# Optimization experiments

Hardware: AMD Instinct MI355X
Metric: run time of the kernel (lower is better)

## Reference

```python
import jax, jax.numpy as jnp
import numpy as np

B, T, C = 2, 2048, 1024
N_HEAD = 16
HEAD_DIM = C // N_HEAD
N_WORLDS = 4


def setup_inputs() -> dict:
    key = jax.random.key(0)
    kx, kq, kk, kv, kp, ka = jax.random.split(key, 6)
    scale = 0.02
    x = jax.random.normal(kx, (B, T, C), dtype=jnp.float32)
    Wq = jax.random.normal(kq, (C, C), dtype=jnp.float32) * scale
    Wk = jax.random.normal(kk, (C, C), dtype=jnp.float32) * scale
    Wv = jax.random.normal(kv, (C, C), dtype=jnp.float32) * scale
    Wproj = jax.random.normal(kp, (C, C), dtype=jnp.float32) * scale
    acc = jax.random.randint(ka, (N_WORLDS, N_WORLDS), 0, 2, dtype=jnp.int32)
    # ensure every world accesses itself so no softmax row is fully masked
    acc = acc.at[jnp.arange(N_WORLDS), jnp.arange(N_WORLDS)].set(1)
    return {"x": x, "Wq": Wq, "Wk": Wk, "Wv": Wv, "Wproj": Wproj,
            "accessibility": acc}


def reference(x, Wq, Wk, Wv, Wproj, accessibility):
    Bd, Td, Cd = x.shape
    # torch Linear: y = x @ W.T  -> project then split heads
    q = (x @ Wq.T).reshape(Bd, Td, N_HEAD, HEAD_DIM).transpose(0, 2, 1, 3)
    k = (x @ Wk.T).reshape(Bd, Td, N_HEAD, HEAD_DIM).transpose(0, 2, 1, 3)
    v = (x @ Wv.T).reshape(Bd, Td, N_HEAD, HEAD_DIM).transpose(0, 2, 1, 3)

    scores = jnp.einsum('bhqd,bhkd->bhqk', q, k) / jnp.sqrt(
        jnp.asarray(HEAD_DIM, dtype=x.dtype))

    # Kripke modal mask: token t lives in world t % n_worlds (necessity: \u25a1)
    world = jnp.arange(Td) % accessibility.shape[0]
    modal_mask = accessibility[world][:, world]          # (T, T) 0/1
    scores = jnp.where(modal_mask[None, None] == 0, -jnp.inf, scores)

    attn = jax.nn.softmax(scores, axis=-1)
    out = jnp.einsum('bhqk,bhkd->bhqd', attn, v)
    out = out.transpose(0, 2, 1, 3).reshape(Bd, Td, Cd)
    return out @ Wproj.T
```

## Files before the change

### kernel.cpp

```cpp
#include <hip/hip_runtime.h>
#include <hip/hip_bf16.h>
#include <stdint.h>


typedef __attribute__((ext_vector_type(8))) __bf16   bf16x8;
typedef __attribute__((ext_vector_type(4))) float    f32x4;
typedef __attribute__((ext_vector_type(8))) ushort   ushort8;

__device__ __forceinline__ ushort f2bf(float x) {
    uint32_t u = __float_as_uint(x);
    return (ushort)((u + 0x7fffu + ((u >> 16) & 1u)) >> 16);
}
__device__ __forceinline__ float sentinel(float v, float s) {
    return (fabsf(v) < 1e30f) ? v : s;
}
__device__ __forceinline__ f32x4 mfma16(bf16x8 a, bf16x8 b, f32x4 c) {
    return __builtin_amdgcn_mfma_f32_16x16x32_bf16(a, b, c, 0, 0, 0);
}
__device__ __forceinline__ ushort2 pk2(float a, float b) {
    __hip_bfloat162 h = __float22bfloat162_rn(make_float2(a, b));
    union { __hip_bfloat162 h; ushort2 u; } c; c.h = h; return c.u;
}
__device__ __forceinline__ ushort4 cvt4(float4 v) {
    ushort2 lo = pk2(v.x, v.y), hi = pk2(v.z, v.w);
    ushort4 r; r.x = lo.x; r.y = lo.y; r.z = hi.x; r.w = hi.y; return r;
}
__device__ __forceinline__ ushort4 cvt4s(float4 v, float s) {
    ushort2 lo = pk2(v.x * s, v.y * s), hi = pk2(v.z * s, v.w * s);
    ushort4 r; r.x = lo.x; r.y = lo.y; r.z = hi.x; r.w = hi.y; return r;
}
__device__ __forceinline__ float fexp2(float x) {
#if __has_builtin(__builtin_amdgcn_exp2f)
    return __builtin_amdgcn_exp2f(x);
#else
    return exp2f(x);
#endif
}
__device__ __forceinline__ void gld16(const ushort* g, ushort* l) {
    auto* g1 = reinterpret_cast<const __attribute__((address_space(1))) uint32_t*>(
        reinterpret_cast<uintptr_t>(g));
    auto* l3 = reinterpret_cast<__attribute__((address_space(3))) uint32_t*>(
        reinterpret_cast<uintptr_t>(l));
    __builtin_amdgcn_global_load_lds(g1, l3, 16, 0, 0);
}

__device__ __forceinline__ int swz(int row, int ch) {
    return row * 64 + ((ch ^ (row & 7)) * 8);
}

__device__ __forceinline__ int wperm(int ts) {
    return ((ts & 3) << 9) | (ts >> 2);
}

__device__ __forceinline__ int vshuf(int r) {
    return ((r & 31) << 2) | (r >> 5);
}
__device__ __forceinline__ int vshufX(int r) {
    return ((r & 63) << 2) | (r >> 6);
}

#define QSCALE 0.1803368801111244f

__global__ __launch_bounds__(256) void cvt_prepass(
        const float* __restrict__ x,  const float* __restrict__ Wq,
        const float* __restrict__ Wk, const float* __restrict__ Wv,
        const float* __restrict__ Wp,
        ushort* __restrict__ xb,  ushort* __restrict__ wqb,
        ushort* __restrict__ wkb, ushort* __restrict__ wvb,
        ushort* __restrict__ wpb)
{
    int gid = blockIdx.x;
    const float* src; ushort* dst; float sc = 1.0f; int boff;
    if (gid < 4096)      { src = x;  dst = xb;  boff = gid; }
    else if (gid < 5120) { src = Wq; dst = wqb; boff = gid - 4096; sc = QSCALE; }
    else if (gid < 6144) { src = Wk; dst = wkb; boff = gid - 5120; }
    else if (gid < 7168) { src = Wv; dst = wvb; boff = gid - 6144; }
    else                 { src = Wp; dst = wpb; boff = gid - 7168; }
    size_t idx = (size_t)boff * 1024 + threadIdx.x * 4;
    float4 v = *(const float4*)&src[idx];
    *(ushort4*)&dst[idx] = cvt4s(v, sc);
}

__global__ __launch_bounds__(512, 2) void gemm_qkv_b(
        const ushort* __restrict__ xb,
        const ushort* __restrict__ wqb, const ushort* __restrict__ wkb,
        const ushort* __restrict__ wvb,
        ushort* __restrict__ Cq, ushort* __restrict__ Ck,
        ushort* __restrict__ Cv)
{
    __shared__ ushort As[2][256 * 32];
    __shared__ ushort Bs[2][256 * 32];

    const int tid  = threadIdx.x;
    const int lane = tid & 63;
    const int wave = tid >> 6;
    const int quad = lane >> 4;
    const int l15  = lane & 15;
    const int wm2  = wave >> 2;
    const int wn4  = wave & 3;

    const int bid = blockIdx.x;
    const bool isV = bid >= 128;
    int tokb, chO;
    const ushort* __restrict__ Aw;
    ushort* __restrict__ C;
    if (!isV) {
        const int blkM = bid & 7;
        const int blkN = bid >> 3;
        tokb = blkN * 256;
        const int chb2 = blkM * 256;
        chO  = chb2 & 1023;
        Aw = (blkM < 4) ? (wqb + (size_t)chb2 * 1024)
                        : (wkb + (size_t)(chb2 - 1024) * 1024);
        C  = (blkM < 4) ? Cq : Ck;
    } else {
        const int v = bid - 128;
        tokb = (v & 15) * 256;
        chO  = (v >> 4) * 256;
        Aw = wvb + (size_t)chO * 1024;
        C  = Cv;
    }

    auto stage = [&](int kt, int buf) {
        const int kcol = kt * 32;
        #pragma unroll
        for (int j = 0; j < 2; ++j) {
            int ci = j * 512 + tid;
            int r  = ci >> 2;
            int qc = (((ci & 3) ^ (r & 3) ^ ((r >> 2) & 3))) * 8;
            const ushort* asrc = isV ? &xb[(size_t)(tokb + vshufX(r)) * 1024]
                                     : &Aw[(size_t)r * 1024];
            const ushort* bsrc = isV ? &Aw[(size_t)r * 1024]
                                     : &xb[(size_t)(tokb + r) * 1024];
            gld16(&asrc[kcol + qc], &As[buf][ci * 8]);
            gld16(&bsrc[kcol + qc], &Bs[buf][ci * 8]);
        }
    };

    f32x4 acc[8][4] = {};

    stage(0, 0);
    for (int t = 0; t < 32; ++t) {
        const int cur = t & 1;
        __syncthreads();
        if (t < 31) stage(t + 1, cur ^ 1);

        bf16x8 af[8], bf[4];
        #pragma unroll
        for (int i = 0; i < 8; ++i) {
            int row = wm2 * 128 + i * 16 + l15;
            int pos = quad ^ (row & 3) ^ ((row >> 2) & 3);
            af[i] = *(const bf16x8*)&As[cur][row * 32 + pos * 8];
        }
        #pragma unroll
        for (int tt = 0; tt < 4; ++tt) {
            int row = wn4 * 64 + tt * 16 + l15;
            int pos = quad ^ (row & 3) ^ ((row >> 2) & 3);
            bf[tt] = *(const bf16x8*)&Bs[cur][row * 32 + pos * 8];
        }
        #pragma unroll
        for (int i = 0; i < 8; ++i)
            #pragma unroll
            for (int tt = 0; tt < 4; ++tt)
                acc[i][tt] = mfma16(af[i], bf[tt], acc[i][tt]);
    }

    if (!isV) {
        #pragma unroll
        for (int i = 0; i < 8; ++i) {
            int ch = chO + wm2 * 128 + i * 16 + quad * 4;
            int hh = ch >> 6, d0 = ch & 63;
            #pragma unroll
            for (int tt = 0; tt < 4; ++tt) {
                int n = tokb + wn4 * 64 + tt * 16 + l15;
                int b = n >> 11, ts = n & 2047;
                ushort4 hv;
                hv.x = f2bf(sentinel(acc[i][tt][0], 1e8f));
                hv.y = f2bf(sentinel(acc[i][tt][1], 1e8f));
                hv.z = f2bf(sentinel(acc[i][tt][2], 1e8f));
                hv.w = f2bf(sentinel(acc[i][tt][3], 1e8f));
                *(ushort4*)&C[((size_t)((b << 4) | hh) * 2048 + wperm(ts)) * 64 + d0] = hv;
            }
        }
    } else {
        const int b = tokb >> 11;
        #pragma unroll
        for (int i = 0; i < 8; ++i) {
            int mi0 = wm2 * 128 + i * 16 + quad * 4;
            int colbase = ((mi0 >> 6) << 9) + ((tokb & 2047) >> 2) + (mi0 & 63);
            #pragma unroll
            for (int tt = 0; tt < 4; ++tt) {
                int n = chO + wn4 * 64 + tt * 16 + l15;
                int hh = n >> 6, d = n & 63;
                ushort4 hv;
                hv.x = f2bf(sentinel(acc[i][tt][0], 1e8f));
                hv.y = f2bf(sentinel(acc[i][tt][1], 1e8f));
                hv.z = f2bf(sentinel(acc[i][tt][2], 1e8f));
                hv.w = f2bf(sentinel(acc[i][tt][3], 1e8f));
                *(ushort4*)&C[((size_t)((b << 4) | hh) * 64 + d) * 2048 + colbase] = hv;
            }
        }
    }
}

__global__ __launch_bounds__(256) void gemm_proj_b(
        const ushort* __restrict__ O, const ushort* __restrict__ wpb,
        float* __restrict__ out)
{
    __shared__ ushort As[128 * 64];
    __shared__ ushort Bs[64 * 64];

    const int lin  = blockIdx.x + 16 * blockIdx.y;
    const int xcd  = lin & 7;
    const int slot = lin >> 3;
    const int bx   = (xcd & 1) * 8 + (slot % 8);
    const int by   = (xcd >> 1) * 8 + (slot / 8);

    const int tid  = threadIdx.x;
    const int lane = tid & 63;
    const int wave = tid >> 6;
    const int quad = lane >> 4;
    const int l15  = lane & 15;
    const int bm = by * 128, bn = bx * 64;
    const int wm = (wave & 1) * 64,  wn = (wave >> 1) * 32;

    f32x4 acc[4][2] = {};

    for (int k0 = 0; k0 < 1024; k0 += 64) {
        __syncthreads();
        int h = k0 >> 6;
        #pragma unroll
        for (int j = 0; j < 4; ++j) {
            int cb = j * 256 + wave * 64;
            int ci = cb + lane;
            int r  = ci >> 3;
            int qc = (ci & 7) ^ (r & 7);
            int m = bm + r;
            int b = m >> 11, ts = m & 2047;
            gld16(&O[((((size_t)(b * 16 + h)) * 2048 + wperm(ts)) << 6) + qc * 8],
                  &As[cb * 8]);
        }
        #pragma unroll
        for (int j = 0; j < 2; ++j) {
            int cb = j * 256 + wave * 64;
            int ci = cb + lane;
            int r  = ci >> 3;
            int qc = (ci & 7) ^ (r & 7);
            gld16(&wpb[(size_t)(bn + r) * 1024 + k0 + qc * 8], &Bs[cb * 8]);
        }
        __syncthreads();

        bf16x8 af[2][4], bfr[2][2];
        #pragma unroll
        for (int f = 0; f < 2; ++f) {
            int ch = f * 4 + quad;
            #pragma unroll
            for (int i = 0; i < 4; ++i)
                af[f][i] = *(const bf16x8*)&As[swz(wm + i * 16 + l15, ch)];
            #pragma unroll
            for (int t = 0; t < 2; ++t)
                bfr[f][t] = *(const bf16x8*)&Bs[swz(wn + t * 16 + l15, ch)];
        }
        #pragma unroll
        for (int f = 0; f < 2; ++f)
            #pragma unroll
            for (int i = 0; i < 4; ++i)
                #pragma unroll
                for (int t = 0; t < 2; ++t)
                    acc[i][t] = mfma16(af[f][i], bfr[f][t], acc[i][t]);
    }

    #pragma unroll
    for (int i = 0; i < 4; ++i)
        #pragma unroll
        for (int t = 0; t < 2; ++t)
            #pragma unroll
            for (int r = 0; r < 4; ++r) {
                int m = bm + wm + i * 16 + quad * 4 + r;
                int n = bn + wn + t * 16 + l15;
                out[(size_t)m * 1024 + n] = sentinel(acc[i][t][r], 100.0f);
            }
}

__global__ __launch_bounds__(256) void attn_kernel(
        ushort* __restrict__ Q, const ushort* __restrict__ Kk,
        const ushort* __restrict__ Vt_g, const int* __restrict__ accm)
{
    __shared__ ushort Ks[2][64 * 64];
    __shared__ ushort Vt[2][64 * 64];
    __shared__ ushort Ps[4][32 * 64];

    const int tid  = threadIdx.x;
    const int lane = tid & 63;
    const int wave = tid >> 6;
    const int quad = lane >> 4;
    const int l15  = lane & 15;
    const int bh = blockIdx.x, qt = blockIdx.y;

    ushort*       Qg = Q    + ((size_t)bh * 2048 + qt * 128) * 64;
    const ushort* Kg = Kk   + (size_t)bh * 2048 * 64;
    const ushort* Vg = Vt_g + (size_t)bh * 64 * 2048;

    const int qworld = qt >> 2;
    int gpack = 0, ng = 0;
    #pragma unroll
    for (int w = 0; w < 4; ++w)
        if (accm[qworld * 4 + w] != 0) { gpack |= w << (ng * 8); ++ng; }
    const int nkt = ng * 8;
    auto ktof = [&](int i) {
        return ((((gpack >> ((i >> 3) << 3)) & 3) << 3) | (i & 7));
    };

    bf16x8 aq[2][2];
    #pragma unroll
    for (int i = 0; i < 2; ++i)
        #pragma unroll
        for (int f = 0; f < 2; ++f)
            aq[i][f] = *(const bf16x8*)
                &Qg[(wave * 32 + i * 16 + l15) * 64 + f * 32 + quad * 8];

    bf16x8 aones;
    #pragma unroll
    for (int j = 0; j < 8; ++j) aones[j] = (__bf16)1.0f;

    f32x4 oacc[4][2] = {};
    f32x4 lacc[2] = {};

    auto stage = [&](int kt, int buf) {
        #pragma unroll
        for (int j = 0; j < 2; ++j) {
            int cb = j * 256 + wave * 64;
            int ci = cb + lane;
            int r  = ci >> 3;
            int qc = (ci & 7) ^ (r & 7);
            gld16(&Kg[((size_t)kt * 64 + r) * 64 + qc * 8], &Ks[buf][cb * 8]);
            gld16(&Vg[(size_t)r * 2048 + kt * 64 + qc * 8], &Vt[buf][cb * 8]);
        }
    };

    stage(ktof(0), 0);
    for (int it = 0; it < nkt; ++it) {
        const int cur = it & 1;
        __syncthreads();
        if (it < nkt - 1) stage(ktof(it + 1), cur ^ 1);

        f32x4 st[4][2] = {};
        #pragma unroll
        for (int f = 0; f < 2; ++f) {
            int ch = f * 4 + quad;
            #pragma unroll
            for (int k4 = 0; k4 < 4; ++k4) {
                bf16x8 ak = *(const bf16x8*)&Ks[cur][swz(k4 * 16 + l15, ch)];
                #pragma unroll
                for (int i = 0; i < 2; ++i)
                    st[k4][i] = mfma16(ak, aq[i][f], st[k4][i]);
            }
        }

        #pragma unroll
        for (int i = 0; i < 2; ++i) {
            int prow = i * 16 + l15;
            #pragma unroll
            for (int k4 = 0; k4 < 4; ++k4) {
                float p0 = fexp2(st[k4][i][0]);
                float p1 = fexp2(st[k4][i][1]);
                float p2 = fexp2(st[k4][i][2]);
                float p3 = fexp2(st[k4][i][3]);
                ushort2 lo = pk2(p0, p1), hi = pk2(p2, p3);
                ushort4 pv4; pv4.x = lo.x; pv4.y = lo.y;
                pv4.z = hi.x; pv4.w = hi.y;
                int pc8 = (k4 * 2 + (quad >> 1)) ^ (l15 & 7);
                *(ushort4*)&Ps[wave][prow * 64 + pc8 * 8 + (quad & 1) * 4] = pv4;
            }
        }

        bf16x8 bp[2][2];
        #pragma unroll
        for (int i = 0; i < 2; ++i)
            #pragma unroll
            for (int f = 0; f < 2; ++f)
                bp[i][f] = *(const bf16x8*)&Ps[wave][swz(i * 16 + l15, f * 4 + quad)];
        #pragma unroll
        for (int f = 0; f < 2; ++f) {
            int ch = f * 4 + quad;
            #pragma unroll
            for (int i = 0; i < 2; ++i)
                lacc[i] = mfma16(aones, bp[i][f], lacc[i]);
            #pragma unroll
            for (int dt = 0; dt < 4; ++dt) {
                bf16x8 av = *(const bf16x8*)&Vt[cur][swz(dt * 16 + l15, ch)];
                #pragma unroll
                for (int i = 0; i < 2; ++i)
                    oacc[dt][i] = mfma16(av, bp[i][f], oacc[dt][i]);
            }
        }
    }

    #pragma unroll
    for (int i = 0; i < 2; ++i) {
        const float inv = 1.0f / lacc[i][0];
        #pragma unroll
        for (int dt = 0; dt < 4; ++dt) {
            ushort4 o4;
            o4.x = f2bf(sentinel(oacc[dt][i][0] * inv, 1e4f));
            o4.y = f2bf(sentinel(oacc[dt][i][1] * inv, 1e4f));
            o4.z = f2bf(sentinel(oacc[dt][i][2] * inv, 1e4f));
            o4.w = f2bf(sentinel(oacc[dt][i][3] * inv, 1e4f));
            *(ushort4*)&Qg[(wave * 32 + i * 16 + l15) * 64 + dt * 16 + quad * 4] = o4;
        }
    }
}

__global__ __launch_bounds__(256) void gemm_qkv_f32(
        const float* __restrict__ A,
        const float* __restrict__ Wq, const float* __restrict__ Wk,
        const float* __restrict__ Wv,
        ushort* __restrict__ Cq, ushort* __restrict__ Ck,
        ushort* __restrict__ Cv)
{
    __shared__ __align__(16) ushort As[128 * 72];
    __shared__ __align__(16) ushort Bs[128 * 72];

    const int sel = blockIdx.x >> 3;
    const float* __restrict__ Bw = sel == 0 ? Wq : (sel == 1 ? Wk : Wv);
    ushort* __restrict__ C       = sel == 0 ? Cq : (sel == 1 ? Ck : Cv);
    const float scale = sel == 0 ? QSCALE : 1.0f;

    const int tid  = threadIdx.x;
    const int lane = tid & 63;
    const int wave = tid >> 6;
    const int quad = lane >> 4;
    const int l15  = lane & 15;
    const int bm = blockIdx.y * 128;
    const int bn = (blockIdx.x & 7) * 128;
    const int wm = (wave & 1) * 64, wn = (wave >> 1) * 64;

    f32x4 acc[4][4] = {};

    for (int k0 = 0; k0 < 1024; k0 += 64) {
        __syncthreads();
        #pragma unroll
        for (int i = 0; i < 8; ++i) {
            int c = tid + 256 * i;
            int row = c >> 4, col = (c & 15) * 4;
            int rg = (sel == 2) ? vshuf(row) : row;
            float4 a4 = *(const float4*)&A[(size_t)(bm + rg) * 1024 + k0 + col];
            *(ushort4*)&As[row * 72 + col] = cvt4(a4);
            float4 b4 = *(const float4*)&Bw[(size_t)(bn + row) * 1024 + k0 + col];
            *(ushort4*)&Bs[row * 72 + col] = cvt4s(b4, scale);
        }
        __syncthreads();

        bf16x8 af[2][4], bfr[2][4];
        #pragma unroll
        for (int f = 0; f < 2; ++f)
            #pragma unroll
            for (int i = 0; i < 4; ++i) {
                af[f][i]  = *(const bf16x8*)&As[(wm + i * 16 + l15) * 72 + f * 32 + quad * 8];
                bfr[f][i] = *(const bf16x8*)&Bs[(wn + i * 16 + l15) * 72 + f * 32 + quad * 8];
            }
        #pragma unroll
        for (int f = 0; f < 2; ++f)
            #pragma unroll
            for (int i = 0; i < 4; ++i)
                #pragma unroll
                for (int t = 0; t < 4; ++t)
                    acc[i][t] = mfma16(af[f][i], bfr[f][t], acc[i][t]);
    }

    if (sel < 2) {
        #pragma unroll
        for (int i = 0; i < 4; ++i)
            #pragma unroll
            for (int t = 0; t < 4; ++t)
                #pragma unroll
                for (int r = 0; r < 4; ++r) {
                    int m = bm + wm + i * 16 + quad * 4 + r;
                    int n = bn + wn + t * 16 + l15;
                    int b = m >> 11, ts = m & 2047, hh = n >> 6, d = n & 63;
                    C[((size_t)((b << 4) | hh) * 2048 + wperm(ts)) * 64 + d] =
                        f2bf(sentinel(acc[i][t][r], 1e8f));
                }
    } else {
        const int b = bm >> 11;
        #pragma unroll
        for (int i = 0; i < 4; ++i) {
            int mi0 = wm + i * 16 + quad * 4;
            int colbase = ((mi0 >> 5) << 9) + ((bm & 2047) >> 2) + (mi0 & 31);
            #pragma unroll
            for (int t = 0; t < 4; ++t) {
                int n = bn + wn + t * 16 + l15;
                int hh = n >> 6, d = n & 63;
                ushort4 hv;
                hv.x = f2bf(sentinel(acc[i][t][0], 1e8f));
                hv.y = f2bf(sentinel(acc[i][t][1], 1e8f));
                hv.z = f2bf(sentinel(acc[i][t][2], 1e8f));
                hv.w = f2bf(sentinel(acc[i][t][3], 1e8f));
                *(ushort4*)&C[((size_t)((b << 4) | hh) * 64 + d) * 2048 + colbase] = hv;
            }
        }
    }
}

__global__ __launch_bounds__(256) void gemm_proj_f32(
        const ushort* __restrict__ A, const float* __restrict__ Bw,
        float* __restrict__ C)
{
    __shared__ __align__(16) ushort As[128 * 72];
    __shared__ __align__(16) ushort Bs[64 * 72];

    const int tid  = threadIdx.x;
    const int lane = tid & 63;
    const int wave = tid >> 6;
    const int quad = lane >> 4;
    const int l15  = lane & 15;
    const int bm = blockIdx.y * 128, bn = blockIdx.x * 64;
    const int wm = (wave & 1) * 64,  wn = (wave >> 1) * 32;

    f32x4 acc[4][2] = {};

    for (int k0 = 0; k0 < 1024; k0 += 64) {
        __syncthreads();
        #pragma unroll
        for (int i = 0; i < 4; ++i) {
            int c = tid + 256 * i;
            int row = c >> 3, col = (c & 7) * 8;
            int m = bm + row;
            int b = m >> 11, ts = m & 2047, h = k0 >> 6;
            size_t aoff = ((((size_t)(b * 16 + h)) * 2048 + wperm(ts)) << 6) + col;
            *(ushort8*)&As[row * 72 + col] = *(const ushort8*)&A[aoff];
        }
        #pragma unroll
        for (int i = 0; i < 4; ++i) {
            int c = tid + 256 * i;
            int row = c >> 4, col = (c & 15) * 4;
            float4 b4 = *(const float4*)&Bw[(size_t)(bn + row) * 1024 + k0 + col];
            *(ushort4*)&Bs[row * 72 + col] = cvt4(b4);
        }
        __syncthreads();

        bf16x8 af[2][4], bfr[2][2];
        #pragma unroll
        for (int f = 0; f < 2; ++f) {
            #pragma unroll
            for (int i = 0; i < 4; ++i)
                af[f][i] = *(const bf16x8*)&As[(wm + i * 16 + l15) * 72 + f * 32 + quad * 8];
            #pragma unroll
            for (int t = 0; t < 2; ++t)
                bfr[f][t] = *(const bf16x8*)&Bs[(wn + t * 16 + l15) * 72 + f * 32 + quad * 8];
        }
        #pragma unroll
        for (int f = 0; f < 2; ++f)
            #pragma unroll
            for (int i = 0; i < 4; ++i)
                #pragma unroll
                for (int t = 0; t < 2; ++t)
                    acc[i][t] = mfma16(af[f][i], bfr[f][t], acc[i][t]);
    }

    #pragma unroll
    for (int i = 0; i < 4; ++i)
        #pragma unroll
        for (int t = 0; t < 2; ++t)
            #pragma unroll
            for (int r = 0; r < 4; ++r) {
                int m = bm + wm + i * 16 + quad * 4 + r;
                int n = bn + wn + t * 16 + l15;
                C[(size_t)m * 1024 + n] = sentinel(acc[i][t][r], 100.0f);
            }
}

__global__ void diag_kernel(float* out, int n, float val) {
    int i = blockIdx.x * blockDim.x + threadIdx.x;
    if (i < n) out[i] = (i == 0) ? val : 0.f;
}

extern "C" void kernel_launch(void* const* d_in, const int* in_sizes, int n_in,
                              void* d_out, int out_size, void* d_ws, size_t ws_size,
                              hipStream_t stream) {
    const float* x  = (const float*)d_in[0];
    const float* Wq = (const float*)d_in[1];
    const float* Wk = (const float*)d_in[2];
    const float* Wv = (const float*)d_in[3];
    const float* Wp = (const float*)d_in[4];
    const int* accm = (const int*)d_in[5];
    float* out = (float*)d_out;

    const size_t SZ = (size_t)4 * 1024 * 1024;
    const size_t WSZ = (size_t)1024 * 1024;

    if (ws_size < 3 * SZ * sizeof(ushort)) {
        diag_kernel<<<(out_size + 255) / 256, 256, 0, stream>>>(
            out, out_size, (float)ws_size);
        return;
    }

    ushort* k_ws = (ushort*)d_ws;
    ushort* v_ws = k_ws + SZ;
    ushort* q_ws = v_ws + SZ;
    dim3 blk(256);

    const size_t need_fast = (4 * SZ + 4 * WSZ) * sizeof(ushort);
    if (ws_size >= need_fast) {
        ushort* xb  = q_ws + SZ;
        ushort* wqb = xb + SZ;
        ushort* wkb = wqb + WSZ;
        ushort* wvb = wkb + WSZ;
        ushort* wpb = wvb + WSZ;
        cvt_prepass<<<8192, blk, 0, stream>>>(x, Wq, Wk, Wv, Wp,
                                              xb, wqb, wkb, wvb, wpb);
        gemm_qkv_b<<<dim3(192), dim3(512), 0, stream>>>(xb, wqb, wkb, wvb,
                                                        q_ws, k_ws, v_ws);
        attn_kernel<<<dim3(32, 16), blk, 0, stream>>>(q_ws, k_ws, v_ws, accm);
        gemm_proj_b<<<dim3(16, 32), blk, 0, stream>>>(q_ws, wpb, out);
    } else {
        gemm_qkv_f32<<<dim3(24, 32), blk, 0, stream>>>(x, Wq, Wk, Wv,
                                                       q_ws, k_ws, v_ws);
        attn_kernel<<<dim3(32, 16), blk, 0, stream>>>(q_ws, k_ws, v_ws, accm);
        gemm_proj_f32<<<dim3(16, 32), blk, 0, stream>>>(q_ws, Wp, out);
    }
}
```

Measured before the change: 163.6 us.

## Triple-buffer QKV GEMM with 64-wide K tiles and swap proj GEMM operands

The QKV GEMM now uses 256x128 output tiles with 64-wide K steps and a three-stage LDS ring, using explicit vmcnt waits, raw barriers and setprio instead of a double-buffered __syncthreads loop. The grid doubles to 384 blocks to improve CU occupancy, at the cost of more LDS per block (about 144KB) and more redundant operand loads. The projection GEMM swaps the A/B roles so each lane writes contiguous float4 chunks of the output instead of scalar stores. The LDS footprint may limit the launch bound of two blocks per CU.

```diff
diff --git a/kernel.cpp b/kernel.cpp
--- a/kernel.cpp
+++ b/kernel.cpp
@@ -88,8 +88,8 @@
         ushort* __restrict__ Cq, ushort* __restrict__ Ck,
         ushort* __restrict__ Cv)
 {
-    __shared__ ushort As[2][256 * 32];
-    __shared__ ushort Bs[2][256 * 32];
+    __shared__ ushort As[3][256 * 64];
+    __shared__ ushort Bs[3][128 * 64];
 
     const int tid  = threadIdx.x;
     const int lane = tid & 63;
@@ -100,69 +100,91 @@
     const int wn4  = wave & 3;
 
     const int bid = blockIdx.x;
-    const bool isV = bid >= 128;
+    const bool isV = bid >= 256;
     int tokb, chO;
-    const ushort* __restrict__ Aw;
+    const ushort* __restrict__ Asrc;
+    const ushort* __restrict__ Bsrc;
     ushort* __restrict__ C;
     if (!isV) {
         const int blkM = bid & 7;
         const int blkN = bid >> 3;
-        tokb = blkN * 256;
+        tokb = blkN * 128;
         const int chb2 = blkM * 256;
         chO  = chb2 & 1023;
-        Aw = (blkM < 4) ? (wqb + (size_t)chb2 * 1024)
-                        : (wkb + (size_t)(chb2 - 1024) * 1024);
-        C  = (blkM < 4) ? Cq : Ck;
+        Asrc = (blkM < 4) ? (wqb + (size_t)chb2 * 1024)
+                          : (wkb + (size_t)(chb2 - 1024) * 1024);
+        Bsrc = xb;
+        C    = (blkM < 4) ? Cq : Ck;
     } else {
-        const int v = bid - 128;
-        tokb = (v & 15) * 256;
-        chO  = (v >> 4) * 256;
-        Aw = wvb + (size_t)chO * 1024;
-        C  = Cv;
+        const int v = bid - 256;
+        const int blkVn = v & 7;
+        tokb = (v >> 3) * 256;
+        chO  = blkVn * 128;
+        Asrc = xb;
+        Bsrc = wvb + (size_t)chO * 1024;
+        C    = Cv;
     }
 
     auto stage = [&](int kt, int buf) {
-        const int kcol = kt * 32;
+        const int kcol = kt * 64;
+        #pragma unroll
+        for (int j = 0; j < 4; ++j) {
+            int ci = j * 512 + tid;
+            int r  = ci >> 3;
+            int qc = ((ci & 7) ^ (r & 7)) * 8;
+            int rg = isV ? (tokb + vshufX(r)) : r;
+            const ushort* src = isV ? &Asrc[(size_t)rg * 1024]
+                                    : &Asrc[(size_t)r * 1024];
+            gld16(&src[kcol + qc], &As[buf][ci * 8]);
+        }
         #pragma unroll
         for (int j = 0; j < 2; ++j) {
             int ci = j * 512 + tid;
-            int r  = ci >> 2;
-            int qc = (((ci & 3) ^ (r & 3) ^ ((r >> 2) & 3))) * 8;
-            const ushort* asrc = isV ? &xb[(size_t)(tokb + vshufX(r)) * 1024]
-                                     : &Aw[(size_t)r * 1024];
-            const ushort* bsrc = isV ? &Aw[(size_t)r * 1024]
-                                     : &xb[(size_t)(tokb + r) * 1024];
-            gld16(&asrc[kcol + qc], &As[buf][ci * 8]);
-            gld16(&bsrc[kcol + qc], &Bs[buf][ci * 8]);
+            int r  = ci >> 3;
+            int qc = ((ci & 7) ^ (r & 7)) * 8;
+            const ushort* src = isV ? &Bsrc[(size_t)r * 1024]
+                                    : &Bsrc[(size_t)(tokb + r) * 1024];
+            gld16(&src[kcol + qc], &Bs[buf][ci * 8]);
         }
     };
 
-    f32x4 acc[8][4] = {};
+    f32x4 acc[8][2] = {};
 
     stage(0, 0);
-    for (int t = 0; t < 32; ++t) {
-        const int cur = t & 1;
-        __syncthreads();
-        if (t < 31) stage(t + 1, cur ^ 1);
-
-        bf16x8 af[8], bf[4];
-        #pragma unroll
-        for (int i = 0; i < 8; ++i) {
-            int row = wm2 * 128 + i * 16 + l15;
-            int pos = quad ^ (row & 3) ^ ((row >> 2) & 3);
-            af[i] = *(const bf16x8*)&As[cur][row * 32 + pos * 8];
-        }
-        #pragma unroll
-        for (int tt = 0; tt < 4; ++tt) {
-            int row = wn4 * 64 + tt * 16 + l15;
-            int pos = quad ^ (row & 3) ^ ((row >> 2) & 3);
-            bf[tt] = *(const bf16x8*)&Bs[cur][row * 32 + pos * 8];
-        }
-        #pragma unroll
-        for (int i = 0; i < 8; ++i)
-            #pragma unroll
-            for (int tt = 0; tt < 4; ++tt)
-                acc[i][tt] = mfma16(af[i], bf[tt], acc[i][tt]);
+    stage(1, 1);
+    asm volatile("s_waitcnt vmcnt(6)" ::: "memory");
+    __builtin_amdgcn_s_barrier();
+    __builtin_amdgcn_sched_barrier(0);
+
+    for (int t = 0; t < 16; ++t) {
+        const int cur = t % 3;
+        if (t + 2 < 16) stage(t + 2, (t + 2) % 3);
+
+        __builtin_amdgcn_s_setprio(1);
+        #pragma unroll
+        for (int f = 0; f < 2; ++f) {
+            int ch = f * 4 + quad;
+            bf16x8 af[8], bfv[2];
+            #pragma unroll
+            for (int i = 0; i < 8; ++i)
+                af[i] = *(const bf16x8*)&As[cur][swz(wm2 * 128 + i * 16 + l15, ch)];
+            #pragma unroll
+            for (int tt = 0; tt < 2; ++tt)
+                bfv[tt] = *(const bf16x8*)&Bs[cur][swz(wn4 * 32 + tt * 16 + l15, ch)];
+            #pragma unroll
+            for (int i = 0; i < 8; ++i)
+                #pragma unroll
+                for (int tt = 0; tt < 2; ++tt)
+                    acc[i][tt] = mfma16(af[i], bfv[tt], acc[i][tt]);
+        }
+        __builtin_amdgcn_s_setprio(0);
+
+        if (t < 15) {
+            if (t < 14) asm volatile("s_waitcnt vmcnt(6)" ::: "memory");
+            else        asm volatile("s_waitcnt vmcnt(0)" ::: "memory");
+            __builtin_amdgcn_s_barrier();
+            __builtin_amdgcn_sched_barrier(0);
+        }
     }
 
     if (!isV) {
@@ -171,8 +193,8 @@
             int ch = chO + wm2 * 128 + i * 16 + quad * 4;
             int hh = ch >> 6, d0 = ch & 63;
             #pragma unroll
-            for (int tt = 0; tt < 4; ++tt) {
-                int n = tokb + wn4 * 64 + tt * 16 + l15;
+            for (int tt = 0; tt < 2; ++tt) {
+                int n = tokb + wn4 * 32 + tt * 16 + l15;
                 int b = n >> 11, ts = n & 2047;
                 ushort4 hv;
                 hv.x = f2bf(sentinel(acc[i][tt][0], 1e8f));
@@ -189,8 +211,8 @@
             int mi0 = wm2 * 128 + i * 16 + quad * 4;
             int colbase = ((mi0 >> 6) << 9) + ((tokb & 2047) >> 2) + (mi0 & 63);
             #pragma unroll
-            for (int tt = 0; tt < 4; ++tt) {
-                int n = chO + wn4 * 64 + tt * 16 + l15;
+            for (int tt = 0; tt < 2; ++tt) {
+                int n = chO + wn4 * 32 + tt * 16 + l15;
                 int hh = n >> 6, d = n & 63;
                 ushort4 hv;
                 hv.x = f2bf(sentinel(acc[i][tt][0], 1e8f));
@@ -207,8 +229,8 @@
         const ushort* __restrict__ O, const ushort* __restrict__ wpb,
         float* __restrict__ out)
 {
-    __shared__ ushort As[128 * 64];
-    __shared__ ushort Bs[64 * 64];
+    __shared__ ushort As[64 * 64];
+    __shared__ ushort Bs[128 * 64];
 
     const int lin  = blockIdx.x + 16 * blockIdx.y;
     const int xcd  = lin & 7;
@@ -221,65 +243,69 @@
     const int wave = tid >> 6;
     const int quad = lane >> 4;
     const int l15  = lane & 15;
-    const int bm = by * 128, bn = bx * 64;
-    const int wm = (wave & 1) * 64,  wn = (wave >> 1) * 32;
-
-    f32x4 acc[4][2] = {};
+    const int chb = bx * 64, tokb = by * 128;
+    const int wm = (wave & 1) * 32,  wn = (wave >> 1) * 64;
+
+    f32x4 acc[2][4] = {};
 
     for (int k0 = 0; k0 < 1024; k0 += 64) {
         __syncthreads();
         int h = k0 >> 6;
+        #pragma unroll
+        for (int j = 0; j < 2; ++j) {
+            int cb = j * 256 + wave * 64;
+            int ci = cb + lane;
+            int r  = ci >> 3;
+            int qc = (ci & 7) ^ (r & 7);
+            gld16(&wpb[(size_t)(chb + r) * 1024 + k0 + qc * 8], &As[cb * 8]);
+        }
         #pragma unroll
         for (int j = 0; j < 4; ++j) {
             int cb = j * 256 + wave * 64;
             int ci = cb + lane;
             int r  = ci >> 3;
             int qc = (ci & 7) ^ (r & 7);
-            int m = bm + r;
+            int m = tokb + r;
             int b = m >> 11, ts = m & 2047;
             gld16(&O[((((size_t)(b * 16 + h)) * 2048 + wperm(ts)) << 6) + qc * 8],
-                  &As[cb * 8]);
-        }
-        #pragma unroll
-        for (int j = 0; j < 2; ++j) {
-            int cb = j * 256 + wave * 64;
-            int ci = cb + lane;
-            int r  = ci >> 3;
-            int qc = (ci & 7) ^ (r & 7);
-            gld16(&wpb[(size_t)(bn + r) * 1024 + k0 + qc * 8], &Bs[cb * 8]);
+                  &Bs[cb * 8]);
         }
         __syncthreads();
 
-        bf16x8 af[2][4], bfr[2][2];
+        bf16x8 af[2][2], bfr[2][4];
         #pragma unroll
         for (int f = 0; f < 2; ++f) {
             int ch = f * 4 + quad;
             #pragma unroll
-            for (int i = 0; i < 4; ++i)
+            for (int i = 0; i < 2; ++i)
                 af[f][i] = *(const bf16x8*)&As[swz(wm + i * 16 + l15, ch)];
             #pragma unroll
-            for (int t = 0; t < 2; ++t)
+            for (int t = 0; t < 4; ++t)
                 bfr[f][t] = *(const bf16x8*)&Bs[swz(wn + t * 16 + l15, ch)];
         }
         #pragma unroll
         for (int f = 0; f < 2; ++f)
             #pragma unroll
-            for (int i = 0; i < 4; ++i)
+            for (int i = 0; i < 2; ++i)
                 #pragma unroll
-                for (int t = 0; t < 2; ++t)
+                for (int t = 0; t < 4; ++t)
                     acc[i][t] = mfma16(af[f][i], bfr[f][t], acc[i][t]);
     }
 
     #pragma unroll
-    for (int i = 0; i < 4; ++i)
-        #pragma unroll
-        for (int t = 0; t < 2; ++t)
-            #pragma unroll
-            for (int r = 0; r < 4; ++r) {
-                int m = bm + wm + i * 16 + quad * 4 + r;
-                int n = bn + wn + t * 16 + l15;
-                out[(size_t)m * 1024 + n] = sentinel(acc[i][t][r], 100.0f);
-            }
+    for (int i = 0; i < 2; ++i) {
+        int n0 = chb + wm + i * 16 + quad * 4;
+        #pragma unroll
+        for (int t = 0; t < 4; ++t) {
+            int m = tokb + wn + t * 16 + l15;
+            float4 v4;
+            v4.x = sentinel(acc[i][t][0], 100.0f);
+            v4.y = sentinel(acc[i][t][1], 100.0f);
+            v4.z = sentinel(acc[i][t][2], 100.0f);
+            v4.w = sentinel(acc[i][t][3], 100.0f);
+            *(float4*)&out[(size_t)m * 1024 + n0] = v4;
+        }
+    }
 }
 
 __global__ __launch_bounds__(256) void attn_kernel(
@@ -609,7 +635,7 @@
         ushort* wpb = wvb + WSZ;
         cvt_prepass<<<8192, blk, 0, stream>>>(x, Wq, Wk, Wv, Wp,
                                               xb, wqb, wkb, wvb, wpb);
-        gemm_qkv_b<<<dim3(192), dim3(512), 0, stream>>>(xb, wqb, wkb, wvb,
+        gemm_qkv_b<<<dim3(384), dim3(512), 0, stream>>>(xb, wqb, wkb, wvb,
                                                         q_ws, k_ws, v_ws);
         attn_kernel<<<dim3(32, 16), blk, 0, stream>>>(q_ws, k_ws, v_ws, accm);
         gemm_proj_b<<<dim3(16, 32), blk, 0, stream>>>(q_ws, wpb, out);
```

After: 167.4 us. 2.3% more time.
